# Optimization experiments

Hardware: AMD Instinct MI355X
Metric: run time of the kernel (lower is better)

## Reference

```python
import jax, jax.numpy as jnp
import numpy as np
from jax import lax

# Model dims (match init_kwargs)
D, K, V, H, R = 256, 16, 64, 4, 23
B, HH, WW = 16, 64, 64
EPS = 1e-5


def setup_inputs() -> dict:
    key = jax.random.key(0)
    ks = jax.random.split(key, 6)
    s = 0.05
    x = jax.random.normal(ks[0], (B, D, HH, WW), dtype=jnp.float32)
    Wq = jax.random.normal(ks[1], (H * K, D), dtype=jnp.float32) * s
    Wk = jax.random.normal(ks[2], (K, D), dtype=jnp.float32) * s
    Wv = jax.random.normal(ks[3], (V, D), dtype=jnp.float32) * s
    conv_w = jax.random.normal(ks[4], (K, 1, R, 1), dtype=jnp.float32) * s  # Conv2d(1, k, (r,1))
    conv_b = jnp.zeros((K,), jnp.float32)
    # BatchNorm (inference-mode) params for query and value branches
    q_gamma = jnp.ones((H * K,), jnp.float32)
    q_beta = jnp.zeros((H * K,), jnp.float32)
    q_mean = jnp.zeros((H * K,), jnp.float32)
    q_var = jnp.ones((H * K,), jnp.float32)
    v_gamma = jnp.ones((V,), jnp.float32)
    v_beta = jnp.zeros((V,), jnp.float32)
    v_mean = jnp.zeros((V,), jnp.float32)
    v_var = jnp.ones((V,), jnp.float32)
    return dict(x=x, Wq=Wq, q_gamma=q_gamma, q_beta=q_beta, q_mean=q_mean, q_var=q_var,
                Wk=Wk, Wv=Wv, v_gamma=v_gamma, v_beta=v_beta, v_mean=v_mean, v_var=v_var,
                conv_w=conv_w, conv_b=conv_b)


def _bn(y, g, b_, m, v_):
    # y: (b, c, n); per-channel affine normalization (eval-mode BatchNorm)
    scale = (g * lax.rsqrt(v_ + EPS))[None, :, None]
    return (y - m[None, :, None]) * scale + b_[None, :, None]


def reference(x, Wq, q_gamma, q_beta, q_mean, q_var, Wk, Wv, v_gamma, v_beta, v_mean, v_var, conv_w, conv_b):
    b, d, h, w = x.shape
    n = h * w
    xf = x.reshape(b, d, n)  # (b, d, n)

    # query: 1x1 conv -> BN -> (b, H, n, K)
    q = _bn(jnp.einsum('od,bdn->bon', Wq, xf), q_gamma, q_beta, q_mean, q_var)
    q = q.reshape(b, H, K, n).transpose(0, 1, 3, 2)  # (b, H, n, K)

    # key: 1x1 conv -> softmax over positions -> (b, n, K)
    kk = jax.nn.softmax(jnp.einsum('od,bdn->bon', Wk, xf), axis=-1).transpose(0, 2, 1)

    # value: 1x1 conv -> BN -> (b, n, V)
    vv = _bn(jnp.einsum('od,bdn->bon', Wv, xf), v_gamma, v_beta, v_mean, v_var).transpose(0, 2, 1)

    # content lambda: (b, K, V)
    lam_c = jnp.einsum('bmk,bmv->bkv', kk, vv)

    # position lambda via local conv over positions: (b, n, K, V)
    pad = (R - 1) // 2
    lam_p = lax.conv_general_dilated(
        vv[:, None, :, :], conv_w, window_strides=(1, 1),
        padding=[(pad, pad), (0, 0)],
        dimension_numbers=('NCHW', 'OIHW', 'NCHW'))  # (b, K, n, V)
    lam_p = lam_p + conv_b[None, :, None, None]
    lam_p = lam_p.transpose(0, 2, 1, 3)  # (b, n, K, V)

    # apply lambdas per position: (b, n, H, V)
    out = jnp.einsum('bhnk,bnkv->bnhv', q, lam_c[:, None, :, :] + lam_p)
    return out.reshape(b, h, w, H * V).transpose(0, 3, 1, 2)  # (b, H*V, h, w)
```

## Files before the change

### kernel.cpp

```cpp
#include <hip/hip_runtime.h>
#include <hip/hip_bf16.h>

typedef unsigned int uint;
typedef unsigned short ushort;

#define Bn 16
#define Dd 256
#define Nn 4096
#define Hh 4
#define Kk 16
#define Vv 64
#define Rr 23
#define Cc 144
#define NRT 9

typedef short bf16x8s __attribute__((ext_vector_type(8)));
typedef float f32x4 __attribute__((ext_vector_type(4)));

static __device__ __forceinline__ ushort f2bf(float f) {
    __hip_bfloat16 h = __float2bfloat16(f);
    return __builtin_bit_cast(ushort, h);
}
static __device__ __forceinline__ float bf2f(ushort u) {
    return __uint_as_float(((uint)u) << 16);
}
static __device__ __forceinline__ float bflo(uint u) { return __uint_as_float(u << 16); }
static __device__ __forceinline__ float bfhi(uint u) { return __uint_as_float(u & 0xffff0000u); }

__global__ __launch_bounds__(256) void pack_kernel(
    const float* __restrict__ Wq, const float* __restrict__ qg, const float* __restrict__ qb,
    const float* __restrict__ qm, const float* __restrict__ qv,
    const float* __restrict__ Wk, const float* __restrict__ Wv,
    const float* __restrict__ vg, const float* __restrict__ vb,
    const float* __restrict__ vm, const float* __restrict__ vvar,
    const float* __restrict__ conv_w,
    ushort* __restrict__ Wf16, float* __restrict__ bias,
    ushort* __restrict__ cwf, float* __restrict__ num, float* __restrict__ den) {
    int c = blockIdx.x;
    int t = threadIdx.x;
    int d = t;
    float scale, bs;
    const float* src;
    if (c < 64) {
        scale = qg[c] * rsqrtf(qv[c] + 1e-5f);
        bs = qb[c] - qm[c] * scale;
        src = Wq + c * Dd;
    } else if (c < 80) {
        scale = 1.f; bs = 0.f;
        src = Wk + (c - 64) * Dd;
    } else {
        int j = c - 80;
        scale = vg[j] * rsqrtf(vvar[j] + 1e-5f);
        bs = vb[j] - vm[j] * scale;
        src = Wv + j * Dd;
    }
    int rt = c >> 4, lm = c & 15;
    int kk = d >> 5, hi = (d >> 3) & 3, j = d & 7;
    Wf16[((rt * 8 + kk) * 64 + hi * 16 + lm) * 8 + j] = f2bf(src[d] * scale);
    if (d == 0) bias[c] = bs;

    if (c == 0) {
#pragma unroll
        for (int m = 0; m < 4; m++) {
            int flat = t + 256 * m;
            int mt = flat >> 9, rem = flat & 511;
            int l = rem >> 3, jj = rem & 7;
            int r = mt * 16 + (l & 15);
            int k = (l >> 4) * 8 + jj;
            float v = (r < Rr && k < Kk) ? conv_w[k * Rr + r] : 0.f;
            cwf[flat] = f2bf(v);
        }
    }
    if (c == 1) {
        float4 z = {0.f, 0.f, 0.f, 0.f};
#pragma unroll
        for (int m = 0; m < 16; m++)
            reinterpret_cast<float4*>(num)[t + 256 * m] = z;
        if (t < 64) reinterpret_cast<float4*>(den)[t] = z;
    }
}

__global__ __launch_bounds__(256, 4) void proj_mfma_kernel(
    const float* __restrict__ x, const ushort* __restrict__ Wf16,
    const float* __restrict__ bias,
    ushort* __restrict__ qbufT, float* __restrict__ kbuf,
    ushort* __restrict__ vbufT) {
    __shared__ ushort Wlds[NRT * 2 * 64 * 8];

    int b = blockIdx.y;
    int n0 = blockIdx.x * 64;
    int t = threadIdx.x;
    int w = t >> 6, l = t & 63;
    int lm = l & 15, hi = l >> 4;
    int n = n0 + w * 16 + lm;

    const uint* WfU = (const uint*)Wf16;
    uint* WldsU = (uint*)Wlds;

    f32x4 acc[NRT];
#pragma unroll
    for (int rt = 0; rt < NRT; rt++) acc[rt] = (f32x4){0.f, 0.f, 0.f, 0.f};

    const float* xb = x + (size_t)b * Dd * Nn + n;

#pragma unroll
    for (int p = 0; p < 4; p++) {
        int kb = p * 2;
        if (p) __syncthreads();
#pragma unroll
        for (int i = 0; i < 18; i++) {
            int flat = t + 256 * i;
            int f2 = flat >> 8;
            int rt = f2 >> 1, kkl = f2 & 1;
            WldsU[flat] = WfU[((rt * 8 + kb + kkl) << 8) + (flat & 255)];
        }
        __syncthreads();

#pragma unroll
        for (int kkl = 0; kkl < 2; kkl++) {
            int kk = kb + kkl;
            const float* xp = xb + (size_t)(kk * 32 + hi * 8) * Nn;
            float f[8];
#pragma unroll
            for (int j = 0; j < 8; j++) f[j] = xp[(size_t)j * Nn];
            bf16x8s bfrag;
#pragma unroll
            for (int j = 0; j < 8; j++) bfrag[j] = (short)f2bf(f[j]);
#pragma unroll
            for (int rt = 0; rt < NRT; rt++) {
                bf16x8s afrag = *reinterpret_cast<const bf16x8s*>(
                    &Wlds[(size_t)((rt * 2 + kkl) * 64 + l) * 8]);
                acc[rt] = __builtin_amdgcn_mfma_f32_16x16x32_bf16(afrag, bfrag, acc[rt], 0, 0, 0);
            }
        }
    }

#pragma unroll
    for (int rr = 0; rr < 4; rr++) {
        int kc = hi * 4 + rr;
        kbuf[((size_t)b * 16 + kc) * Nn + n] = acc[4][rr] + bias[64 + kc];
    }

    __syncthreads();
    {
        int nl = w * 16 + lm;
#pragma unroll
        for (int rt = 0; rt < 4; rt++)
#pragma unroll
            for (int rr = 0; rr < 4; rr++) {
                int kq = hi * 4 + rr;
                Wlds[nl * 72 + kq * 4 + rt] = f2bf(acc[rt][rr] + bias[rt * 16 + kq]);
            }
#pragma unroll
        for (int rt = 5; rt < 9; rt++)
#pragma unroll
            for (int rr = 0; rr < 4; rr++) {
                int v = (rt - 5) * 16 + hi * 4 + rr;
                Wlds[4608 + nl * 72 + v] = f2bf(acc[rt][rr] + bias[80 + v]);
            }
    }
    __syncthreads();

#pragma unroll
    for (int m = 0; m < 2; m++) {
        int i = t + 256 * m;
        int row = i >> 3, seg = i & 7;
        uint4 u = *reinterpret_cast<const uint4*>(&Wlds[row * 72 + seg * 8]);
        *reinterpret_cast<uint4*>(&qbufT[((size_t)b * Nn + n0 + row) * 64 + seg * 8]) = u;
    }
#pragma unroll
    for (int m = 0; m < 2; m++) {
        int i = t + 256 * m;
        int row = i >> 3, seg = i & 7;
        uint4 u = *reinterpret_cast<const uint4*>(&Wlds[4608 + row * 72 + seg * 8]);
        *reinterpret_cast<uint4*>(&vbufT[((size_t)b * Nn + n0 + row) * 64 + seg * 8]) = u;
    }
}

#define NCHUNK 128
__global__ __launch_bounds__(256) void lamc_kernel(
    const float* __restrict__ kbuf, const ushort* __restrict__ vbufT,
    float* __restrict__ num, float* __restrict__ den) {
    int b = blockIdx.y;
    int n0 = blockIdx.x * NCHUNK;
    __shared__ float kks[Kk][NCHUNK + 1];
    __shared__ ushort vvT[NCHUNK][72];
    __shared__ float dpart[Kk][32];
    int t = threadIdx.x;
#pragma unroll
    for (int m = 0; m < 2; m++) {
        int i = t + 256 * m;
        int r = i >> 5, seg = i & 31;
        float4 f = *reinterpret_cast<const float4*>(&kbuf[((size_t)b * 16 + r) * Nn + n0 + seg * 4]);
        float e0 = __expf(f.x), e1 = __expf(f.y), e2 = __expf(f.z), e3 = __expf(f.w);
        kks[r][seg * 4 + 0] = e0;
        kks[r][seg * 4 + 1] = e1;
        kks[r][seg * 4 + 2] = e2;
        kks[r][seg * 4 + 3] = e3;
        dpart[r][seg] = e0 + e1 + e2 + e3;
    }
#pragma unroll
    for (int m = 0; m < 4; m++) {
        int i = t + 256 * m;
        int row = i >> 3, seg = i & 7;
        uint4 u = *reinterpret_cast<const uint4*>(&vbufT[((size_t)b * Nn + n0 + row) * 64 + seg * 8]);
        *reinterpret_cast<uint4*>(&vvT[row][seg * 8]) = u;
    }
    __syncthreads();
    int v = t & 63, k0 = t >> 6;
    float acc4[4] = {0.f, 0.f, 0.f, 0.f};
    for (int nl = 0; nl < NCHUNK; nl++) {
        float wv = bf2f(vvT[nl][v]);
#pragma unroll
        for (int j2 = 0; j2 < 4; j2++) acc4[j2] += kks[k0 + 4 * j2][nl] * wv;
    }
#pragma unroll
    for (int j2 = 0; j2 < 4; j2++)
        atomicAdd(&num[((size_t)b * Kk + k0 + 4 * j2) * Vv + v], acc4[j2]);
    if (t < Kk) {
        float s = 0.f;
#pragma unroll
        for (int seg = 0; seg < 32; seg++) s += dpart[t][seg];
        atomicAdd(&den[(size_t)b * Kk + t], s);
    }
}

#define TN 32
__global__ __launch_bounds__(256, 4) void fused_out_kernel(
    const ushort* __restrict__ qbufT, const ushort* __restrict__ vbufT,
    const ushort* __restrict__ cwf, const float* __restrict__ num,
    const float* __restrict__ den, const float* __restrict__ conv_b,
    float* __restrict__ out) {
    __shared__ ushort Af[12 * 64 * 8];
    __shared__ ushort Sf[4][12 * 32 * 8];
    __shared__ ushort Qf[4][2 * 64 * 8];

    int b = blockIdx.y;
    int n0 = blockIdx.x * TN;
    int t = threadIdx.x;
    int l = t & 63;

    uint4 vld0 = {0, 0, 0, 0}, vld1 = {0, 0, 0, 0};
    {
        int c = t >> 3, vg = t & 7;
        int n = n0 - 11 + c;
        if (n >= 0 && n < Nn)
            vld0 = *reinterpret_cast<const uint4*>(&vbufT[((size_t)b * Nn + n) * 64 + vg * 8]);
        int i2 = t + 256;
        if (i2 < 432) {
            int c2 = i2 >> 3, vg2 = i2 & 7;
            int n2 = n0 - 11 + c2;
            if (n2 >= 0 && n2 < Nn)
                vld1 = *reinterpret_cast<const uint4*>(&vbufT[((size_t)b * Nn + n2) * 64 + vg2 * 8]);
        }
    }
    uint2 qld0, qld1;
    {
        int i = t;
        qld0 = *reinterpret_cast<const uint2*>(
            &qbufT[((size_t)b * Nn + n0 + (i & 31)) * 64 + (i >> 5) * 4]);
        int i2 = t + 256;
        qld1 = *reinterpret_cast<const uint2*>(
            &qbufT[((size_t)b * Nn + n0 + (i2 & 31)) * 64 + (i2 >> 5) * 4]);
    }
    uint4 cwld0 = *reinterpret_cast<const uint4*>(&cwf[(0 * 64 + l) * 8]);
    uint4 cwld1 = *reinterpret_cast<const uint4*>(&cwf[(1 * 64 + l) * 8]);
    float4 lcl = *reinterpret_cast<const float4*>(&num[(size_t)b * Kk * Vv + t * 4]);
    float dk = den[(size_t)b * Kk + (t >> 4)];
    float cb = conv_b[t >> 4];

    uint4 z4 = {0, 0, 0, 0};
#pragma unroll
    for (int m = 0; m < 3; m++) reinterpret_cast<uint4*>(Af)[t + 256 * m] = z4;
#pragma unroll
    for (int m = 0; m < 6; m++) reinterpret_cast<uint4*>(Sf)[t + 256 * m] = z4;
#pragma unroll
    for (int m = 0; m < 2; m++) reinterpret_cast<uint4*>(Qf)[t + 256 * m] = z4;
    __syncthreads();

    {
        int c = t >> 3, vg = t & 7;
        int kk = c >> 5, hi = (c >> 3) & 3, j = c & 7;
        ushort* base = &Af[((kk * 4 + hi) * 64 + vg * 8) * 8 + j];
        uint va[4] = {vld0.x, vld0.y, vld0.z, vld0.w};
#pragma unroll
        for (int e = 0; e < 4; e++) {
            base[(2 * e + 0) * 8] = (ushort)(va[e] & 0xffff);
            base[(2 * e + 1) * 8] = (ushort)(va[e] >> 16);
        }
        int i2 = t + 256;
        if (i2 < 432) {
            int c2 = i2 >> 3, vg2 = i2 & 7;
            int kk2 = c2 >> 5, hi2 = (c2 >> 3) & 3, j2 = c2 & 7;
            ushort* base2 = &Af[((kk2 * 4 + hi2) * 64 + vg2 * 8) * 8 + j2];
            uint vb4[4] = {vld1.x, vld1.y, vld1.z, vld1.w};
#pragma unroll
            for (int e = 0; e < 4; e++) {
                base2[(2 * e + 0) * 8] = (ushort)(vb4[e] & 0xffff);
                base2[(2 * e + 1) * 8] = (ushort)(vb4[e] >> 16);
            }
        }
    }
    {
        int k = t >> 4, v0 = (t & 15) * 4;
        int c = 54 + k;
        int kk = c >> 5, hi = (c >> 3) & 3, j = c & 7;
        ushort* base = &Af[((kk * 4 + hi) * 64 + v0) * 8 + j];
        float inv = 1.f / dk;
        base[0]  = f2bf(lcl.x * inv + cb);
        base[8]  = f2bf(lcl.y * inv + cb);
        base[16] = f2bf(lcl.z * inv + cb);
        base[24] = f2bf(lcl.w * inv + cb);
    }
    {
        int i = t;
        {
            int k = i >> 5, nl = i & 31, m = 54 + k;
            int kk = m >> 5, hi = (m >> 3) & 3, j = m & 7;
            int off = ((kk * 4 + hi) * 32 + nl) * 8 + j;
            Sf[0][off] = (ushort)(qld0.x & 0xffff);
            Sf[1][off] = (ushort)(qld0.x >> 16);
            Sf[2][off] = (ushort)(qld0.y & 0xffff);
            Sf[3][off] = (ushort)(qld0.y >> 16);
            int nt = nl >> 4, lmq = nl & 15;
            int qoff = (nt * 64 + (k >> 3) * 16 + lmq) * 8 + (k & 7);
            Qf[0][qoff] = (ushort)(qld0.x & 0xffff);
            Qf[1][qoff] = (ushort)(qld0.x >> 16);
            Qf[2][qoff] = (ushort)(qld0.y & 0xffff);
            Qf[3][qoff] = (ushort)(qld0.y >> 16);
        }
        int i2 = t + 256;
        {
            int k = i2 >> 5, nl = i2 & 31, m = 54 + k;
            int kk = m >> 5, hi = (m >> 3) & 3, j = m & 7;
            int off = ((kk * 4 + hi) * 32 + nl) * 8 + j;
            Sf[0][off] = (ushort)(qld1.x & 0xffff);
            Sf[1][off] = (ushort)(qld1.x >> 16);
            Sf[2][off] = (ushort)(qld1.y & 0xffff);
            Sf[3][off] = (ushort)(qld1.y >> 16);
            int nt = nl >> 4, lmq = nl & 15;
            int qoff = (nt * 64 + (k >> 3) * 16 + lmq) * 8 + (k & 7);
            Qf[0][qoff] = (ushort)(qld1.x & 0xffff);
            Qf[1][qoff] = (ushort)(qld1.x >> 16);
            Qf[2][qoff] = (ushort)(qld1.y & 0xffff);
            Qf[3][qoff] = (ushort)(qld1.y >> 16);
        }
    }
    __syncthreads();

    int h = t >> 6;
    int lm = l & 15, hif = l >> 4;
    {
        bf16x8s cwfr0 = __builtin_bit_cast(bf16x8s, cwld0);
        bf16x8s cwfr1 = __builtin_bit_cast(bf16x8s, cwld1);
        f32x4 gacc[2][2];
#pragma unroll
        for (int nt = 0; nt < 2; nt++) {
            bf16x8s qfr = *reinterpret_cast<const bf16x8s*>(&Qf[h][(nt * 64 + l) * 8]);
            gacc[0][nt] = __builtin_amdgcn_mfma_f32_16x16x32_bf16(
                cwfr0, qfr, (f32x4){0.f, 0.f, 0.f, 0.f}, 0, 0, 0);
            gacc[1][nt] = __builtin_amdgcn_mfma_f32_16x16x32_bf16(
                cwfr1, qfr, (f32x4){0.f, 0.f, 0.f, 0.f}, 0, 0, 0);
        }
#pragma unroll
        for (int mt = 0; mt < 2; mt++)
#pragma unroll
            for (int nt = 0; nt < 2; nt++)
#pragma unroll
                for (int rr = 0; rr < 4; rr++) {
                    int r = mt * 16 + hif * 4 + rr;
                    if (r < Rr) {
                        int nl2 = nt * 16 + lm;
                        int m = nl2 + r;
                        Sf[h][((m >> 3) * 32 + nl2) * 8 + (m & 7)] = f2bf(gacc[mt][nt][rr]);
                    }
                }
    }
    __syncthreads();

    f32x4 acc[4][2];
#pragma unroll
    for (int mt = 0; mt < 4; mt++)
#pragma unroll
        for (int nt = 0; nt < 2; nt++) acc[mt][nt] = (f32x4){0.f, 0.f, 0.f, 0.f};

#pragma unroll
    for (int kk = 0; kk < 3; kk++) {
        bf16x8s bfr[2];
#pragma unroll
        for (int nt = 0; nt < 2; nt++)
            bfr[nt] = *reinterpret_cast<const bf16x8s*>(
                &Sf[h][((kk * 4 + hif) * 32 + nt * 16 + lm) * 8]);
#pragma unroll
        for (int mt = 0; mt < 4; mt++) {
            bf16x8s afr = *reinterpret_cast<const bf16x8s*>(
                &Af[((kk * 4 + hif) * 64 + mt * 16 + lm) * 8]);
#pragma unroll
            for (int nt = 0; nt < 2; nt++)
                acc[mt][nt] = __builtin_amdgcn_mfma_f32_16x16x32_bf16(afr, bfr[nt], acc[mt][nt], 0, 0, 0);
        }
    }

    float* ob = out + ((size_t)b * 256 + h * 64) * Nn + n0;
#pragma unroll
    for (int mt = 0; mt < 4; mt++)
#pragma unroll
        for (int nt = 0; nt < 2; nt++)
#pragma unroll
            for (int rr = 0; rr < 4; rr++) {
                int v = mt * 16 + hif * 4 + rr;
                ob[(size_t)v * Nn + nt * 16 + lm] = acc[mt][nt][rr];
            }
}

extern "C" void kernel_launch(void* const* d_in, const int* in_sizes, int n_in,
                              void* d_out, int out_size, void* d_ws, size_t ws_size,
                              hipStream_t stream) {
    const float* x      = (const float*)d_in[0];
    const float* Wq     = (const float*)d_in[1];
    const float* qg     = (const float*)d_in[2];
    const float* qb     = (const float*)d_in[3];
    const float* qm     = (const float*)d_in[4];
    const float* qv     = (const float*)d_in[5];
    const float* Wk     = (const float*)d_in[6];
    const float* Wv     = (const float*)d_in[7];
    const float* vg     = (const float*)d_in[8];
    const float* vb     = (const float*)d_in[9];
    const float* vm     = (const float*)d_in[10];
    const float* vvar   = (const float*)d_in[11];
    const float* conv_w = (const float*)d_in[12];
    const float* conv_b = (const float*)d_in[13];
    float* out = (float*)d_out;

    float* wsf = (float*)d_ws;
    ushort* Wf16  = (ushort*)wsf;
    float*  bias  = wsf + 18432;
    float*  kbuf  = wsf + 18688;
    float*  num   = wsf + 1067264;
    float*  den   = wsf + 1083648;
    ushort* cwf   = (ushort*)(wsf + 1083904);
    ushort* qbufT = (ushort*)(wsf + 1084928);
    ushort* vbufT = (ushort*)(wsf + 3182080);

    pack_kernel<<<Cc, 256, 0, stream>>>(Wq, qg, qb, qm, qv, Wk, Wv, vg, vb, vm, vvar,
                                        conv_w, Wf16, bias, cwf, num, den);
    proj_mfma_kernel<<<dim3(Nn / 64, Bn), 256, 0, stream>>>(x, Wf16, bias,
                                                            qbufT, kbuf, vbufT);
    lamc_kernel<<<dim3(Nn / NCHUNK, Bn), 256, 0, stream>>>(kbuf, vbufT, num, den);
    fused_out_kernel<<<dim3(Nn / TN, Bn), 256, 0, stream>>>(qbufT, vbufT, cwf, num, den,
                                                            conv_b, out);
}
```

Before: 55.40 us.

## Fuse content-lambda reduction into projection kernel and drop key buffer

```diff
diff --git a/kernel.cpp b/kernel.cpp
--- a/kernel.cpp
+++ b/kernel.cpp
@@ -83,8 +83,8 @@
 __global__ __launch_bounds__(256, 4) void proj_mfma_kernel(
     const float* __restrict__ x, const ushort* __restrict__ Wf16,
     const float* __restrict__ bias,
-    ushort* __restrict__ qbufT, float* __restrict__ kbuf,
-    ushort* __restrict__ vbufT) {
+    ushort* __restrict__ qbufT, ushort* __restrict__ vbufT,
+    float* __restrict__ num, float* __restrict__ den) {
     __shared__ ushort Wlds[NRT * 2 * 64 * 8];
 
     int b = blockIdx.y;
@@ -135,12 +135,6 @@
         }
     }
 
-#pragma unroll
-    for (int rr = 0; rr < 4; rr++) {
-        int kc = hi * 4 + rr;
-        kbuf[((size_t)b * 16 + kc) * Nn + n] = acc[4][rr] + bias[64 + kc];
-    }
-
     __syncthreads();
     {
         int nl = w * 16 + lm;
@@ -175,53 +169,38 @@
         uint4 u = *reinterpret_cast<const uint4*>(&Wlds[4608 + row * 72 + seg * 8]);
         *reinterpret_cast<uint4*>(&vbufT[((size_t)b * Nn + n0 + row) * 64 + seg * 8]) = u;
     }
-}
-
-#define NCHUNK 128
-__global__ __launch_bounds__(256) void lamc_kernel(
-    const float* __restrict__ kbuf, const ushort* __restrict__ vbufT,
-    float* __restrict__ num, float* __restrict__ den) {
-    int b = blockIdx.y;
-    int n0 = blockIdx.x * NCHUNK;
-    __shared__ float kks[Kk][NCHUNK + 1];
-    __shared__ ushort vvT[NCHUNK][72];
-    __shared__ float dpart[Kk][32];
-    int t = threadIdx.x;
-#pragma unroll
-    for (int m = 0; m < 2; m++) {
-        int i = t + 256 * m;
-        int r = i >> 5, seg = i & 31;
-        float4 f = *reinterpret_cast<const float4*>(&kbuf[((size_t)b * 16 + r) * Nn + n0 + seg * 4]);
-        float e0 = __expf(f.x), e1 = __expf(f.y), e2 = __expf(f.z), e3 = __expf(f.w);
-        kks[r][seg * 4 + 0] = e0;
-        kks[r][seg * 4 + 1] = e1;
-        kks[r][seg * 4 + 2] = e2;
-        kks[r][seg * 4 + 3] = e3;
-        dpart[r][seg] = e0 + e1 + e2 + e3;
-    }
-#pragma unroll
-    for (int m = 0; m < 4; m++) {
-        int i = t + 256 * m;
-        int row = i >> 3, seg = i & 7;
-        uint4 u = *reinterpret_cast<const uint4*>(&vbufT[((size_t)b * Nn + n0 + row) * 64 + seg * 8]);
-        *reinterpret_cast<uint4*>(&vvT[row][seg * 8]) = u;
-    }
-    __syncthreads();
-    int v = t & 63, k0 = t >> 6;
-    float acc4[4] = {0.f, 0.f, 0.f, 0.f};
-    for (int nl = 0; nl < NCHUNK; nl++) {
-        float wv = bf2f(vvT[nl][v]);
-#pragma unroll
-        for (int j2 = 0; j2 < 4; j2++) acc4[j2] += kks[k0 + 4 * j2][nl] * wv;
-    }
-#pragma unroll
-    for (int j2 = 0; j2 < 4; j2++)
-        atomicAdd(&num[((size_t)b * Kk + k0 + 4 * j2) * Vv + v], acc4[j2]);
-    if (t < Kk) {
-        float s = 0.f;
-#pragma unroll
-        for (int seg = 0; seg < 32; seg++) s += dpart[t][seg];
-        atomicAdd(&den[(size_t)b * Kk + t], s);
+
+    float ev[4];
+#pragma unroll
+    for (int rr = 0; rr < 4; rr++)
+        ev[rr] = __expf(acc[4][rr] + bias[64 + hi * 4 + rr]);
+    __syncthreads();
+    float* eks = reinterpret_cast<float*>(Wlds);
+    {
+        int nl = w * 16 + lm;
+#pragma unroll
+        for (int rr = 0; rr < 4; rr++)
+            eks[(hi * 4 + rr) * 64 + nl] = ev[rr];
+    }
+    __syncthreads();
+    {
+        int v = t & 63, k0 = t >> 6;
+        float a4[4] = {0.f, 0.f, 0.f, 0.f};
+        for (int nl = 0; nl < 64; nl++) {
+            float wv = bf2f(Wlds[4608 + nl * 72 + v]);
+#pragma unroll
+            for (int j2 = 0; j2 < 4; j2++)
+                a4[j2] += eks[(k0 + 4 * j2) * 64 + nl] * wv;
+        }
+#pragma unroll
+        for (int j2 = 0; j2 < 4; j2++)
+            atomicAdd(&num[((size_t)b * Kk + k0 + 4 * j2) * Vv + v], a4[j2]);
+        if (t < Kk) {
+            float s = 0.f;
+#pragma unroll
+            for (int nl = 0; nl < 64; nl++) s += eks[t * 64 + nl];
+            atomicAdd(&den[(size_t)b * Kk + t], s);
+        }
     }
 }
 
@@ -435,18 +414,16 @@
     float* wsf = (float*)d_ws;
     ushort* Wf16  = (ushort*)wsf;
     float*  bias  = wsf + 18432;
-    float*  kbuf  = wsf + 18688;
-    float*  num   = wsf + 1067264;
-    float*  den   = wsf + 1083648;
-    ushort* cwf   = (ushort*)(wsf + 1083904);
-    ushort* qbufT = (ushort*)(wsf + 1084928);
-    ushort* vbufT = (ushort*)(wsf + 3182080);
+    float*  num   = wsf + 18688;
+    float*  den   = wsf + 35072;
+    ushort* cwf   = (ushort*)(wsf + 35328);
+    ushort* qbufT = (ushort*)(wsf + 35840);
+    ushort* vbufT = (ushort*)(wsf + 2132992);
 
     pack_kernel<<<Cc, 256, 0, stream>>>(Wq, qg, qb, qm, qv, Wk, Wv, vg, vb, vm, vvar,
                                         conv_w, Wf16, bias, cwf, num, den);
     proj_mfma_kernel<<<dim3(Nn / 64, Bn), 256, 0, stream>>>(x, Wf16, bias,
-                                                            qbufT, kbuf, vbufT);
-    lamc_kernel<<<dim3(Nn / NCHUNK, Bn), 256, 0, stream>>>(kbuf, vbufT, num, den);
+                                                            qbufT, vbufT, num, den);
     fused_out_kernel<<<dim3(Nn / TN, Bn), 256, 0, stream>>>(qbufT, vbufT, cwf, num, den,
                                                             conv_b, out);
 }
```

Result: faster. 50.01 us (-9.7%).
